# Optimization experiments

Hardware: AMD Instinct MI355X
Metric: run time of the kernel (lower is better)

Reference implementation:

```python
import jax, jax.numpy as jnp
import numpy as np


def setup_inputs() -> dict:
    key = jax.random.key(0)
    k1, k2 = jax.random.split(key)
    pred = jax.random.normal(k1, (4, 4096, 3), dtype=jnp.float32)
    gt = jax.random.normal(k2, (4, 4096, 3), dtype=jnp.float32)
    return {"pred": pred, "gt": gt}


def reference(pred, gt):
    # Chamfer distance with L1 (Manhattan) point-to-point distance.
    # pred: [B, N, 3], gt: [B, M, 3]
    # d[b, n, m] = sum_c |pred[b,n,c] - gt[b,m,c]|
    d = jnp.abs(pred[:, :, None, :] - gt[:, None, :, :]).sum(-1)  # [B, N, M]
    cham_x = d.min(axis=2).mean(axis=1)  # nearest gt for each pred point, [B]
    cham_y = d.min(axis=1).mean(axis=1)  # nearest pred for each gt point, [B]
    # point_reduction='mean' per direction, batch_reduction='mean' (pytorch3d default)
    return jnp.mean(cham_x + cham_y)
```

## Files before the change

### kernel.cpp

```cpp
#include <hip/hip_runtime.h>
#include <cfloat>


constexpr int TPB = 256;
constexpr int PTS = 8;
constexpr int NC  = TPB * PTS;
constexpr int MC  = 64;

__global__ __launch_bounds__(TPB) void chamfer_partial_kernel(
    const float* __restrict__ pred, const float* __restrict__ gt,
    float* __restrict__ partial, int B, int N, int M) {
    const int dir = blockIdx.z;
    const int b   = blockIdx.y;
    const float* q = dir ? gt   : pred;
    const float* t = dir ? pred : gt;
    const int Nq   = dir ? M : N;
    const int Nt   = dir ? N : M;
    const int nchunks = Nq / NC;
    const int nc = blockIdx.x % nchunks;
    const int mc = blockIdx.x / nchunks;

    __shared__ float4 lds4[MC];

    const float* tbase = t + ((size_t)b * Nt + (size_t)mc * MC) * 3;
    for (int i = threadIdx.x; i < MC * 3; i += TPB) {
        ((float*)&lds4[i / 3])[i % 3] = tbase[i];
    }
    __syncthreads();

    const float* qb = q + (size_t)b * Nq * 3;
    float px[PTS], py[PTS], pz[PTS], mn[PTS];
#pragma unroll
    for (int i = 0; i < PTS; ++i) {
        const int n = nc * NC + threadIdx.x + i * TPB;
        px[i] = qb[n * 3 + 0];
        py[i] = qb[n * 3 + 1];
        pz[i] = qb[n * 3 + 2];
        mn[i] = FLT_MAX;
    }

#pragma unroll 8
    for (int j = 0; j < MC; ++j) {
        float4 g = lds4[j];
#pragma unroll
        for (int i = 0; i < PTS; ++i) {
            float d = fabsf(px[i] - g.x) + fabsf(py[i] - g.y) + fabsf(pz[i] - g.z);
            mn[i] = fminf(mn[i], d);
        }
    }

    float* outp = partial + (((size_t)mc * 2 + dir) * B + b) * N + nc * NC + threadIdx.x;
#pragma unroll
    for (int i = 0; i < PTS; ++i) outp[i * TPB] = mn[i];
}

__global__ __launch_bounds__(256) void chamfer_reduce_kernel(
    const float* __restrict__ partial, float* __restrict__ out,
    int Q, float inv) {
    const int qidx = blockIdx.x * 256 + threadIdx.x;
    float mn = FLT_MAX;
#pragma unroll
    for (int mc = 0; mc < 64; ++mc)
        mn = fminf(mn, partial[(size_t)mc * Q + qidx]);
    float v = mn * inv;

    for (int off = 32; off > 0; off >>= 1) v += __shfl_down(v, off, 64);
    __shared__ float red[4];
    const int lane = threadIdx.x & 63, w = threadIdx.x >> 6;
    if (lane == 0) red[w] = v;
    __syncthreads();
    if (threadIdx.x == 0)
        atomicAdd(out, red[0] + red[1] + red[2] + red[3]);
}

extern "C" void kernel_launch(void* const* d_in, const int* in_sizes, int n_in,
                              void* d_out, int out_size, void* d_ws, size_t ws_size,
                              hipStream_t stream) {
    const float* pred = (const float*)d_in[0];
    const float* gt   = (const float*)d_in[1];
    float* out = (float*)d_out;

    const int B = 4;
    const int N = in_sizes[0] / (B * 3);
    const int M = in_sizes[1] / (B * 3);

    float* partial = (float*)d_ws;
    const int nmc = M / MC;
    const int Q = 2 * B * N;

    hipMemsetAsync(out, 0, sizeof(float), stream);

    dim3 grid((N / NC) * nmc, B, 2);
    chamfer_partial_kernel<<<grid, TPB, 0, stream>>>(pred, gt, partial, B, N, M);

    chamfer_reduce_kernel<<<Q / 256, 256, 0, stream>>>(
        partial, out, Q, 1.0f / (float)(B * N));
}
```

Measured before the change: 79.78 us.

## Enlarge tiles, use SoA shared layout and inline-asm abs-add/min3 inner loop

Doubles points per thread and the target chunk size, and stores target coordinates in LDS as three separate arrays so each iteration reads four targets per coordinate with vector loads. The inner distance computation uses inline assembly that folds absolute values into add operand modifiers and combines minima with v_min3, which reduces VALU instruction count per pair. The grid gets smaller (about 4x fewer blocks) and the reduce kernel reads half as many partials. The risks are higher register pressure and lower occupancy or parallelism on a large GPU.

```diff
diff --git a/kernel.cpp b/kernel.cpp
--- a/kernel.cpp
+++ b/kernel.cpp
@@ -3,9 +3,9 @@
 
 
 constexpr int TPB = 256;
-constexpr int PTS = 8;
+constexpr int PTS = 16;
 constexpr int NC  = TPB * PTS;
-constexpr int MC  = 64;
+constexpr int MC  = 128;
 
 __global__ __launch_bounds__(TPB) void chamfer_partial_kernel(
     const float* __restrict__ pred, const float* __restrict__ gt,
@@ -20,11 +20,14 @@
     const int nc = blockIdx.x % nchunks;
     const int mc = blockIdx.x / nchunks;
 
-    __shared__ float4 lds4[MC];
+    __shared__ __align__(16) float ldsx[MC];
+    __shared__ __align__(16) float ldsy[MC];
+    __shared__ __align__(16) float ldsz[MC];
 
     const float* tbase = t + ((size_t)b * Nt + (size_t)mc * MC) * 3;
     for (int i = threadIdx.x; i < MC * 3; i += TPB) {
-        ((float*)&lds4[i / 3])[i % 3] = tbase[i];
+        const int c = i % 3, p = i / 3;
+        (c == 0 ? ldsx : c == 1 ? ldsy : ldsz)[p] = tbase[i];
     }
     __syncthreads();
 
@@ -39,13 +42,28 @@
         mn[i] = FLT_MAX;
     }
 
-#pragma unroll 8
-    for (int j = 0; j < MC; ++j) {
-        float4 g = lds4[j];
+#pragma unroll 2
+    for (int j = 0; j < MC; j += 4) {
+        float4 gx = *(const float4*)&ldsx[j];
+        float4 gy = *(const float4*)&ldsy[j];
+        float4 gz = *(const float4*)&ldsz[j];
 #pragma unroll
         for (int i = 0; i < PTS; ++i) {
-            float d = fabsf(px[i] - g.x) + fabsf(py[i] - g.y) + fabsf(pz[i] - g.z);
-            mn[i] = fminf(mn[i], d);
+            float dx0 = px[i] - gx.x, dy0 = py[i] - gy.x, dz0 = pz[i] - gz.x;
+            float dx1 = px[i] - gx.y, dy1 = py[i] - gy.y, dz1 = pz[i] - gz.y;
+            float dx2 = px[i] - gx.z, dy2 = py[i] - gy.z, dz2 = pz[i] - gz.z;
+            float dx3 = px[i] - gx.w, dy3 = py[i] - gy.w, dz3 = pz[i] - gz.w;
+            float s0, s1, s2, s3, d0, d1, d2, d3;
+            asm("v_add_f32_e64 %0, |%1|, |%2|" : "=v"(s0) : "v"(dx0), "v"(dy0));
+            asm("v_add_f32_e64 %0, %1, |%2|"   : "=v"(d0) : "v"(s0),  "v"(dz0));
+            asm("v_add_f32_e64 %0, |%1|, |%2|" : "=v"(s1) : "v"(dx1), "v"(dy1));
+            asm("v_add_f32_e64 %0, %1, |%2|"   : "=v"(d1) : "v"(s1),  "v"(dz1));
+            asm("v_add_f32_e64 %0, |%1|, |%2|" : "=v"(s2) : "v"(dx2), "v"(dy2));
+            asm("v_add_f32_e64 %0, %1, |%2|"   : "=v"(d2) : "v"(s2),  "v"(dz2));
+            asm("v_add_f32_e64 %0, |%1|, |%2|" : "=v"(s3) : "v"(dx3), "v"(dy3));
+            asm("v_add_f32_e64 %0, %1, |%2|"   : "=v"(d3) : "v"(s3),  "v"(dz3));
+            asm("v_min3_f32 %0, %0, %1, %2"    : "+v"(mn[i]) : "v"(d0), "v"(d1));
+            asm("v_min3_f32 %0, %0, %1, %2"    : "+v"(mn[i]) : "v"(d2), "v"(d3));
         }
     }
 
@@ -60,7 +78,7 @@
     const int qidx = blockIdx.x * 256 + threadIdx.x;
     float mn = FLT_MAX;
 #pragma unroll
-    for (int mc = 0; mc < 64; ++mc)
+    for (int mc = 0; mc < 32; ++mc)
         mn = fminf(mn, partial[(size_t)mc * Q + qidx]);
     float v = mn * inv;
 
@@ -85,12 +103,11 @@
     const int M = in_sizes[1] / (B * 3);
 
     float* partial = (float*)d_ws;
-    const int nmc = M / MC;
     const int Q = 2 * B * N;
 
     hipMemsetAsync(out, 0, sizeof(float), stream);
 
-    dim3 grid((N / NC) * nmc, B, 2);
+    dim3 grid((N / NC) * (M / MC), B, 2);
     chamfer_partial_kernel<<<grid, TPB, 0, stream>>>(pred, gt, partial, B, N, M);
 
     chamfer_reduce_kernel<<<Q / 256, 256, 0, stream>>>(
```

Result: slower. 84.45 us (+5.9%).
